# Kernel tuning notes

Measured on AMD Instinct MI355X. Metric: run time of the kernel, lower is better.

The kernel has to match this reference:

```python
import jax, jax.numpy as jnp
import numpy as np

B, T, D = 2, 2048, 2048
H, KV = 16, 4
HD = D // H  # 128
ROPE_BASE = 10000.0


def _rope(t):
    # t: [B, h, T, HD]; faithful to torch apply_rope (even/odd split, concat halves)
    pos = jnp.arange(T, dtype=t.dtype)
    inv_freq = 1.0 / (ROPE_BASE ** (jnp.arange(0, HD, 2, dtype=t.dtype) / HD))
    ang = jnp.einsum('t,f->tf', pos, inv_freq)  # [T, HD/2]
    sin = jnp.sin(ang)[None, None]
    cos = jnp.cos(ang)[None, None]
    t1, t2 = t[..., ::2], t[..., 1::2]
    return jnp.concatenate([t1 * cos - t2 * sin, t1 * sin + t2 * cos], axis=-1)


def setup_inputs() -> dict:
    key = jax.random.key(0)
    kx, kq, kk, kv, ko = jax.random.split(key, 5)
    x = jax.random.normal(kx, (B, T, D), dtype=jnp.float32)
    s = 0.02
    Wq = jax.random.normal(kq, (D, D), dtype=jnp.float32) * s
    Wk = jax.random.normal(kk, (D, KV * HD), dtype=jnp.float32) * s
    Wv = jax.random.normal(kv, (D, KV * HD), dtype=jnp.float32) * s
    Wo = jax.random.normal(ko, (D, D), dtype=jnp.float32) * s
    return {"x": x, "Wq": Wq, "Wk": Wk, "Wv": Wv, "Wo": Wo}


def reference(x, Wq, Wk, Wv, Wo):
    # projections (nn.Linear, no bias)
    q = (x @ Wq).reshape(B, T, H, HD).transpose(0, 2, 1, 3)    # [B,H,T,HD]
    k = (x @ Wk).reshape(B, T, KV, HD).transpose(0, 2, 1, 3)   # [B,KV,T,HD]
    v = (x @ Wv).reshape(B, T, KV, HD).transpose(0, 2, 1, 3)
    q = _rope(q)
    k = _rope(k)
    # GQA: repeat_interleave kv heads to full head count
    g = H // KV
    k = jnp.repeat(k, g, axis=1)
    v = jnp.repeat(v, g, axis=1)
    # causal SDPA, default scale 1/sqrt(head_dim)
    scale = 1.0 / jnp.sqrt(jnp.array(HD, dtype=x.dtype))
    scores = jnp.einsum('bhqd,bhkd->bhqk', q, k) * scale
    mask = jnp.tril(jnp.ones((T, T), dtype=bool))
    scores = jnp.where(mask, scores, jnp.finfo(scores.dtype).min)
    attn = jax.nn.softmax(scores, axis=-1)
    out = jnp.einsum('bhqk,bhkd->bhqd', attn, v)               # [B,H,T,HD]
    out = out.transpose(0, 2, 1, 3).reshape(B, T, D)
    return out @ Wo
```

## Files before the change

### kernel.cpp

```cpp
#include <hip/hip_runtime.h>
#include <math.h>

#define BB 2
#define TT 2048
#define DD 2048
#define HH 16
#define KVHN 4
#define HDIM 128
#define NKV 3072

typedef unsigned short u16;
typedef unsigned int u32;
typedef __bf16 bf16x8 __attribute__((ext_vector_type(8)));
typedef float  f32x4  __attribute__((ext_vector_type(4)));

#define AS1 __attribute__((address_space(1)))
#define AS3 __attribute__((address_space(3)))

__device__ __forceinline__ void dma16(const u16* g, u16* l) {
  __builtin_amdgcn_global_load_lds((const AS1 u32*)g, (AS3 u32*)l, 16, 0, 0);
}

__device__ __forceinline__ u16 f2bf(float f) {
  u32 u = __float_as_uint(f);
  u32 r = (u + 0x7FFFu + ((u >> 16) & 1u)) >> 16;
  return (u16)r;
}
__device__ __forceinline__ float bf2f(u32 h) { return __uint_as_float(h << 16); }

__device__ __forceinline__ u32 pack2(float a, float b) {
  union { __bf16 h[2]; u32 u; } cv;
  cv.h[0] = (__bf16)a; cv.h[1] = (__bf16)b;
  return cv.u;
}

__global__ __launch_bounds__(256) void castf2b(const float* __restrict__ in,
                                               u16* __restrict__ out) {
  size_t i4 = (size_t)blockIdx.x * 256 + threadIdx.x;
  float4 v = *(const float4*)(in + i4 * 4);
  ushort4 o;
  o.x = f2bf(v.x); o.y = f2bf(v.y); o.z = f2bf(v.z); o.w = f2bf(v.w);
  *(ushort4*)(out + i4 * 4) = o;
}

__global__ __launch_bounds__(256) void tcast(const float* __restrict__ W,
                                             u16* __restrict__ WT,
                                             int K, int N) {
  __shared__ float tile[32][33];
  const int n0 = blockIdx.x * 32, k0 = blockIdx.y * 32;
  const int r = threadIdx.x >> 3;
  const int c4 = (threadIdx.x & 7) * 4;
  float4 v = *(const float4*)(W + (size_t)(k0 + r) * N + n0 + c4);
  tile[r][c4 + 0] = v.x; tile[r][c4 + 1] = v.y;
  tile[r][c4 + 2] = v.z; tile[r][c4 + 3] = v.w;
  __syncthreads();
  ushort4 o;
  o.x = f2bf(tile[c4 + 0][r]); o.y = f2bf(tile[c4 + 1][r]);
  o.z = f2bf(tile[c4 + 2][r]); o.w = f2bf(tile[c4 + 3][r]);
  *(ushort4*)(WT + (size_t)(n0 + r) * K + k0 + c4) = o;
}

template <int OUT_BF16>
__global__ __launch_bounds__(256) void gemm2(const u16* __restrict__ A,
                                             const u16* __restrict__ BT,
                                             void* __restrict__ Cv,
                                             int N, int K) {
  __shared__ u16 As[128 * 32];
  __shared__ u16 Bs[128 * 32];
  const int t = threadIdx.x;
  const int l = t & 63, w = t >> 6;
  const int lm = l & 15, quad = l >> 4;
  const int wm = w & 1, wn = w >> 1;
  const int m0 = blockIdx.y * 128, n0 = blockIdx.x * 128;
  const int wu = __builtin_amdgcn_readfirstlane(w);

  f32x4 acc[4][4];
  #pragma unroll
  for (int i = 0; i < 4; ++i)
    #pragma unroll
    for (int j = 0; j < 4; ++j) acc[i][j] = (f32x4){0.f, 0.f, 0.f, 0.f};

  for (int k0 = 0; k0 < K; k0 += 32) {
    __syncthreads();
    #pragma unroll
    for (int i = 0; i < 2; ++i) {
      int p0 = (wu * 2 + i) * 64;
      int p = p0 + l;
      int row = p >> 2, c = p & 3;
      dma16(A  + (size_t)(m0 + row) * K + k0 + c * 8, &As[p0 * 8]);
      dma16(BT + (size_t)(n0 + row) * K + k0 + c * 8, &Bs[p0 * 8]);
    }
    __syncthreads();
    bf16x8 a[4], bq[4];
    #pragma unroll
    for (int i = 0; i < 4; ++i)
      a[i] = *(const bf16x8*)&As[(wm * 64 + i * 16 + lm) * 32 + quad * 8];
    #pragma unroll
    for (int j = 0; j < 4; ++j)
      bq[j] = *(const bf16x8*)&Bs[(wn * 64 + j * 16 + lm) * 32 + quad * 8];
    #pragma unroll
    for (int i = 0; i < 4; ++i)
      #pragma unroll
      for (int j = 0; j < 4; ++j)
        acc[i][j] = __builtin_amdgcn_mfma_f32_16x16x32_bf16(a[i], bq[j], acc[i][j], 0, 0, 0);
  }

  #pragma unroll
  for (int i = 0; i < 4; ++i) {
    #pragma unroll
    for (int r = 0; r < 4; ++r) {
      size_t gr = (size_t)(m0 + wm * 64 + i * 16 + quad * 4 + r);
      #pragma unroll
      for (int j = 0; j < 4; ++j) {
        int gc = n0 + wn * 64 + j * 16 + lm;
        if (OUT_BF16) ((u16*)Cv)[gr * N + gc] = f2bf(acc[i][j][r]);
        else          ((float*)Cv)[gr * N + gc] = acc[i][j][r];
      }
    }
  }
}

__global__ __launch_bounds__(256) void rope2(u16* p) {
  const int row = blockIdx.x;
  const int pos = row & (TT - 1);
  u16* base = p + (size_t)row * NKV;
  float e0[5], e1[5];
  #pragma unroll
  for (int i = 0; i < 5; ++i) {
    int item = threadIdx.x + i * 256;
    int h20 = item >> 6, f = item & 63;
    int col = (h20 < 16) ? h20 * 128 : 2048 + (h20 - 16) * 128;
    u32 u = *(const u32*)(base + col + 2 * f);
    e0[i] = bf2f(u & 0xffffu);
    e1[i] = bf2f(u >> 16);
  }
  __syncthreads();
  #pragma unroll
  for (int i = 0; i < 5; ++i) {
    int item = threadIdx.x + i * 256;
    int h20 = item >> 6, f = item & 63;
    int col = (h20 < 16) ? h20 * 128 : 2048 + (h20 - 16) * 128;
    float sc = (h20 < 16) ? 0.08838834764831845f : 1.0f;
    float inv = exp2f((float)f * -0.20762050593046898f);
    float ang = (float)pos * inv;
    float sn = sinf(ang), cs = cosf(ang);
    base[col + f]      = f2bf((e0[i] * cs - e1[i] * sn) * sc);
    base[col + 64 + f] = f2bf((e0[i] * sn + e1[i] * cs) * sc);
  }
}

__global__ __launch_bounds__(256) void vtrans(const u16* __restrict__ QKV,
                                              u16* __restrict__ Vt) {
  __shared__ u16 tl[64][72];
  const int t0 = blockIdx.x * 64;
  const int y  = blockIdx.y;
  const int b  = blockIdx.z;
  #pragma unroll
  for (int i = 0; i < 2; ++i) {
    int idx = threadIdx.x + i * 256;
    int r = idx >> 3, c = (idx & 7) * 8;
    *(uint4*)&tl[r][c] =
        *(const uint4*)(QKV + (size_t)(b * TT + t0 + r) * NKV + 2560 + y * 64 + c);
  }
  __syncthreads();
  const int vh = y >> 1;
  #pragma unroll
  for (int i = 0; i < 2; ++i) {
    int idx = threadIdx.x + i * 256;
    int dr = idx >> 3, tc = (idx & 7) * 8;
    u16 tmp[8];
    #pragma unroll
    for (int j = 0; j < 8; ++j) tmp[j] = tl[tc + j][dr];
    int dloc = (y & 1) * 64 + dr;
    *(uint4*)(Vt + (size_t)((b * KVHN + vh) * HDIM + dloc) * TT + t0 + tc) =
        *(const uint4*)tmp;
  }
}

__global__ __launch_bounds__(256, 2) void attn2(const u16* __restrict__ QKV,
                                                const u16* __restrict__ Vt,
                                                u16* __restrict__ Ob) {
  __shared__ u16 KsA[64 * 128], KsB[64 * 128];
  __shared__ u16 VsA[128 * 64], VsB[128 * 64];
  __shared__ u16 Pw[4 * 2048];
  const int t = threadIdx.x;
  const int l = t & 63, w = t >> 6;
  const int lm = l & 15, quad = l >> 4;
  const int px = blockIdx.x, h = blockIdx.y, b = blockIdx.z;
  const int kvh = h >> 2;
  const int qlo = px * 64, qhi = (31 - px) * 64;
  const int last = 31 - px;
  const int wu = __builtin_amdgcn_readfirstlane(w);
  u16* pwv = &Pw[w * 2048];
  constexpr float L2E = 1.4426950408889634f;

  bf16x8 qf[2][4];
  {
    size_t r0 = (size_t)(b * TT + qlo + w * 16 + lm) * NKV + h * HDIM;
    size_t r1 = (size_t)(b * TT + qhi + w * 16 + lm) * NKV + h * HDIM;
    #pragma unroll
    for (int ks = 0; ks < 4; ++ks) {
      qf[0][ks] = *(const bf16x8*)(QKV + r0 + ks * 32 + quad * 8);
      qf[1][ks] = *(const bf16x8*)(QKV + r1 + ks * 32 + quad * 8);
    }
  }

  f32x4 o[8][2];
  #pragma unroll
  for (int i = 0; i < 8; ++i)
    #pragma unroll
    for (int n = 0; n < 2; ++n) o[i][n] = (f32x4){0.f, 0.f, 0.f, 0.f};
  float m_[2] = {-1e30f, -1e30f}, l_[2] = {0.f, 0.f};

  auto stageK = [&](int kt, u16* dst) {
    #pragma unroll
    for (int i = 0; i < 4; ++i) {
      int p0 = (wu * 4 + i) * 64;
      int p = p0 + l;
      int row = p >> 4, cp = p & 15, cl = cp ^ (row & 15);
      dma16(QKV + (size_t)(b * TT + kt * 64 + row) * NKV + 2048 + kvh * HDIM + cl * 8,
            dst + p0 * 8);
    }
  };
  auto stageV = [&](int kt, u16* dst) {
    #pragma unroll
    for (int i = 0; i < 4; ++i) {
      int p0 = (wu * 4 + i) * 64;
      int p = p0 + l;
      int d = p >> 3, cp = p & 7, cl = cp ^ (d & 7);
      dma16(Vt + (size_t)((b * KVHN + kvh) * HDIM + d) * TT + kt * 64 + cl * 8,
            dst + p0 * 8);
    }
  };

  auto body = [&](int kt, u16* kcur, u16* vcur, u16* knext, u16* vnext) {
    __syncthreads();
    const bool pf = kt < last;
    if (pf) stageV(kt + 1, vnext);
    const bool lo = (kt <= px);

    f32x4 s[4][2];
    #pragma unroll
    for (int mt = 0; mt < 4; ++mt) {
      s[mt][0] = (f32x4){0.f, 0.f, 0.f, 0.f};
      s[mt][1] = (f32x4){0.f, 0.f, 0.f, 0.f};
    }
    #pragma unroll
    for (int ks = 0; ks < 4; ++ks) {
      #pragma unroll
      for (int mt = 0; mt < 4; ++mt) {
        bf16x8 kb = *(const bf16x8*)&kcur[(mt * 16 + lm) * 128 + (((ks * 4 + quad) ^ lm) * 8)];
        if (lo) s[mt][0] = __builtin_amdgcn_mfma_f32_16x16x32_bf16(kb, qf[0][ks], s[mt][0], 0, 0, 0);
        s[mt][1] = __builtin_amdgcn_mfma_f32_16x16x32_bf16(kb, qf[1][ks], s[mt][1], 0, 0, 0);
      }
    }
    if (pf) stageK(kt + 1, knext);

    if (kt == px) {
      #pragma unroll
      for (int mt = 0; mt < 4; ++mt)
        #pragma unroll
        for (int r = 0; r < 4; ++r) {
          int kv = kt * 64 + mt * 16 + quad * 4 + r;
          if (kv > qlo + w * 16 + lm) s[mt][0][r] = -1e30f;
        }
    }
    if (kt == last) {
      #pragma unroll
      for (int mt = 0; mt < 4; ++mt)
        #pragma unroll
        for (int r = 0; r < 4; ++r) {
          int kv = kt * 64 + mt * 16 + quad * 4 + r;
          if (kv > qhi + w * 16 + lm) s[mt][1][r] = -1e30f;
        }
    }

    float al[2] = {1.f, 1.f};
    #pragma unroll
    for (int nt = 0; nt < 2; ++nt) {
      if (nt == 0 && !lo) continue;
      float mx = -1e30f;
      #pragma unroll
      for (int mt = 0; mt < 4; ++mt)
        #pragma unroll
        for (int r = 0; r < 4; ++r) mx = fmaxf(mx, s[mt][nt][r]);
      mx = fmaxf(mx, __shfl_xor(mx, 16));
      mx = fmaxf(mx, __shfl_xor(mx, 32));
      float mn = fmaxf(m_[nt], mx);
      al[nt] = exp2f((m_[nt] - mn) * L2E);
      m_[nt] = mn;
      float sum = 0.f;
      #pragma unroll
      for (int mt = 0; mt < 4; ++mt)
        #pragma unroll
        for (int r = 0; r < 4; ++r) {
          float pv = exp2f((s[mt][nt][r] - mn) * L2E);
          s[mt][nt][r] = pv;
          sum += pv;
        }
      sum += __shfl_xor(sum, 16);
      sum += __shfl_xor(sum, 32);
      l_[nt] = l_[nt] * al[nt] + sum;

      #pragma unroll
      for (int mt = 0; mt < 4; ++mt) {
        u32 p01 = pack2(s[mt][nt][0], s[mt][nt][1]);
        u32 p23 = pack2(s[mt][nt][2], s[mt][nt][3]);
        int phys = (mt * 2 + (quad >> 1)) ^ (lm & 7);
        int addr = (nt * 16 + lm) * 64 + phys * 8 + (quad & 1) * 4;
        uint2 uv; uv.x = p01; uv.y = p23;
        *(uint2*)&pwv[addr] = uv;
      }
      if (__any(al[nt] < 1.0f)) {
        #pragma unroll
        for (int mt2 = 0; mt2 < 8; ++mt2)
          #pragma unroll
          for (int r = 0; r < 4; ++r) o[mt2][nt][r] *= al[nt];
      }
    }

    #pragma unroll
    for (int ks2 = 0; ks2 < 2; ++ks2) {
      int coff = ((ks2 * 4 + quad) ^ (lm & 7)) * 8;
      bf16x8 pb0, pb1;
      if (lo) pb0 = *(const bf16x8*)&pwv[lm * 64 + coff];
      pb1 = *(const bf16x8*)&pwv[(16 + lm) * 64 + coff];
      #pragma unroll
      for (int mt2 = 0; mt2 < 8; ++mt2) {
        bf16x8 vb = *(const bf16x8*)&vcur[(mt2 * 16 + lm) * 64 + coff];
        if (lo) o[mt2][0] = __builtin_amdgcn_mfma_f32_16x16x32_bf16(vb, pb0, o[mt2][0], 0, 0, 0);
        o[mt2][1] = __builtin_amdgcn_mfma_f32_16x16x32_bf16(vb, pb1, o[mt2][1], 0, 0, 0);
      }
    }
  };

  stageK(0, KsA); stageV(0, VsA);
  for (int kt = 0; kt <= last; ++kt) {
    if ((kt & 1) == 0) body(kt, KsA, VsA, KsB, VsB);
    else               body(kt, KsB, VsB, KsA, VsA);
  }

  #pragma unroll
  for (int nt = 0; nt < 2; ++nt) {
    float inv = 1.f / l_[nt];
    #pragma unroll
    for (int mt2 = 0; mt2 < 8; ++mt2) {
      u32 a0 = pack2(o[mt2][nt][0] * inv, o[mt2][nt][1] * inv);
      u32 a1 = pack2(o[mt2][nt][2] * inv, o[mt2][nt][3] * inv);
      int phys = (mt2 * 2 + (quad >> 1)) ^ (lm & 7);
      int addr = lm * 128 + phys * 8 + (quad & 1) * 4;
      uint2 uv; uv.x = a0; uv.y = a1;
      *(uint2*)&pwv[addr] = uv;
    }
    int qt0 = nt ? qhi : qlo;
    #pragma unroll
    for (int i = 0; i < 4; ++i) {
      int p = i * 64 + l;
      int row = p >> 4, cl = p & 15;
      int cph = cl ^ (row & 7);
      uint4 val = *(const uint4*)&pwv[row * 128 + cph * 8];
      *(uint4*)(Ob + (size_t)(b * TT + qt0 + w * 16 + row) * DD + h * HDIM + cl * 8) = val;
    }
  }
}

extern "C" void kernel_launch(void* const* d_in, const int* in_sizes, int n_in,
                              void* d_out, int out_size, void* d_ws, size_t ws_size,
                              hipStream_t stream) {
  const float* x  = (const float*)d_in[0];
  const float* Wq = (const float*)d_in[1];
  const float* Wk = (const float*)d_in[2];
  const float* Wv = (const float*)d_in[3];
  const float* Wo = (const float*)d_in[4];
  float* out = (float*)d_out;

  u16* xb    = (u16*)d_ws;
  u16* WqkvT = xb + 8388608;
  u16* WoT   = xb + 14680064;
  u16* Vt    = WqkvT;
  u16* Ob    = xb;
  u16* QKVb  = (u16*)d_out;

  dim3 blk(256);
  castf2b<<<8192, blk, 0, stream>>>(x, xb);
  tcast<<<dim3(64, 64), blk, 0, stream>>>(Wq, WqkvT, DD, DD);
  tcast<<<dim3(16, 64), blk, 0, stream>>>(Wk, WqkvT + (size_t)2048 * DD, DD, 512);
  tcast<<<dim3(16, 64), blk, 0, stream>>>(Wv, WqkvT + (size_t)2560 * DD, DD, 512);
  tcast<<<dim3(64, 64), blk, 0, stream>>>(Wo, WoT, DD, DD);

  gemm2<1><<<dim3(NKV / 128, 32), blk, 0, stream>>>(xb, WqkvT, QKVb, NKV, DD);
  rope2<<<BB * TT, blk, 0, stream>>>(QKVb);
  vtrans<<<dim3(32, 8, BB), blk, 0, stream>>>(QKVb, Vt);
  attn2<<<dim3(16, HH, BB), blk, 0, stream>>>(QKVb, Vt, Ob);
  gemm2<0><<<dim3(DD / 128, 32), blk, 0, stream>>>(Ob, WoT, out, DD, DD);
}
```

Before: 333.3 us.

## Restructure attention to one q-tile per block with smaller KV tiles

Replaces the paired low/high q-tile attention kernel with one that processes a single 64-row q tile per block, using 32-row KV tiles and smaller shared buffers so four blocks can reside per CU. Block-to-q-tile mapping is staggered by head to balance causal work. It also adds a lazy max-rescale threshold, MFMA priority hints, precomputed DMA pointers, and sincosf in rope. The aim is higher occupancy and better latency hiding, traded against more blocks with unequal work and more barriers per processed key.

```diff
diff --git a/kernel.cpp b/kernel.cpp
--- a/kernel.cpp
+++ b/kernel.cpp
@@ -143,7 +143,8 @@
     float sc = (h20 < 16) ? 0.08838834764831845f : 1.0f;
     float inv = exp2f((float)f * -0.20762050593046898f);
     float ang = (float)pos * inv;
-    float sn = sinf(ang), cs = cosf(ang);
+    float sn, cs;
+    sincosf(ang, &sn, &cs);
     base[col + f]      = f2bf((e0[i] * cs - e1[i] * sn) * sc);
     base[col + 64 + f] = f2bf((e0[i] * sn + e1[i] * cs) * sc);
   }
@@ -177,190 +178,176 @@
   }
 }
 
-__global__ __launch_bounds__(256, 2) void attn2(const u16* __restrict__ QKV,
+__global__ __launch_bounds__(256, 4) void attn3(const u16* __restrict__ QKV,
                                                 const u16* __restrict__ Vt,
                                                 u16* __restrict__ Ob) {
-  __shared__ u16 KsA[64 * 128], KsB[64 * 128];
-  __shared__ u16 VsA[128 * 64], VsB[128 * 64];
-  __shared__ u16 Pw[4 * 2048];
+  __shared__ u16 KsA[32 * 128], KsB[32 * 128];
+  __shared__ u16 VsA[128 * 32], VsB[128 * 32];
+  __shared__ u16 Pw[4 * 512];
   const int t = threadIdx.x;
   const int l = t & 63, w = t >> 6;
   const int lm = l & 15, quad = l >> 4;
-  const int px = blockIdx.x, h = blockIdx.y, b = blockIdx.z;
+  const int h = blockIdx.y, b = blockIdx.z;
+  const int qbase = (blockIdx.x + (blockIdx.y & 7)) & 31;
+  const int qt = (blockIdx.y & 8) ? (31 - qbase) : qbase;
   const int kvh = h >> 2;
-  const int qlo = px * 64, qhi = (31 - px) * 64;
-  const int last = 31 - px;
+  const int q0 = qt * 64;
+  const int last = 2 * qt + 1;
   const int wu = __builtin_amdgcn_readfirstlane(w);
-  u16* pwv = &Pw[w * 2048];
+  u16* pwv = &Pw[w * 512];
   constexpr float L2E = 1.4426950408889634f;
 
-  bf16x8 qf[2][4];
+  bf16x8 qf[4];
   {
-    size_t r0 = (size_t)(b * TT + qlo + w * 16 + lm) * NKV + h * HDIM;
-    size_t r1 = (size_t)(b * TT + qhi + w * 16 + lm) * NKV + h * HDIM;
-    #pragma unroll
-    for (int ks = 0; ks < 4; ++ks) {
-      qf[0][ks] = *(const bf16x8*)(QKV + r0 + ks * 32 + quad * 8);
-      qf[1][ks] = *(const bf16x8*)(QKV + r1 + ks * 32 + quad * 8);
-    }
-  }
-
-  f32x4 o[8][2];
-  #pragma unroll
-  for (int i = 0; i < 8; ++i)
-    #pragma unroll
-    for (int n = 0; n < 2; ++n) o[i][n] = (f32x4){0.f, 0.f, 0.f, 0.f};
-  float m_[2] = {-1e30f, -1e30f}, l_[2] = {0.f, 0.f};
-
-  auto stageK = [&](int kt, u16* dst) {
-    #pragma unroll
-    for (int i = 0; i < 4; ++i) {
-      int p0 = (wu * 4 + i) * 64;
-      int p = p0 + l;
-      int row = p >> 4, cp = p & 15, cl = cp ^ (row & 15);
-      dma16(QKV + (size_t)(b * TT + kt * 64 + row) * NKV + 2048 + kvh * HDIM + cl * 8,
-            dst + p0 * 8);
-    }
-  };
-  auto stageV = [&](int kt, u16* dst) {
-    #pragma unroll
-    for (int i = 0; i < 4; ++i) {
-      int p0 = (wu * 4 + i) * 64;
-      int p = p0 + l;
-      int d = p >> 3, cp = p & 7, cl = cp ^ (d & 7);
-      dma16(Vt + (size_t)((b * KVHN + kvh) * HDIM + d) * TT + kt * 64 + cl * 8,
-            dst + p0 * 8);
-    }
-  };
-
-  auto body = [&](int kt, u16* kcur, u16* vcur, u16* knext, u16* vnext) {
+    size_t r0 = (size_t)(b * TT + q0 + w * 16 + lm) * NKV + h * HDIM;
+    #pragma unroll
+    for (int ks = 0; ks < 4; ++ks)
+      qf[ks] = *(const bf16x8*)(QKV + r0 + ks * 32 + quad * 8);
+  }
+
+  f32x4 o[8];
+  #pragma unroll
+  for (int i = 0; i < 8; ++i) o[i] = (f32x4){0.f, 0.f, 0.f, 0.f};
+  float m_ = -1e30f, l_ = 0.f;
+
+  const u16 *kg[2], *vg[2];
+  int koff[2], voff[2];
+  #pragma unroll
+  for (int i = 0; i < 2; ++i) {
+    int p0 = (wu * 2 + i) * 64, p = p0 + l;
+    int krow = p >> 4, kcp = p & 15, kcl = kcp ^ (krow & 15);
+    kg[i] = QKV + (size_t)(b * TT + krow) * NKV + 2048 + kvh * HDIM + kcl * 8;
+    koff[i] = p0 * 8;
+    int vd = p >> 2, vcp = p & 3, vcl = vcp ^ (vd & 3);
+    vg[i] = Vt + (size_t)((b * KVHN + kvh) * HDIM + vd) * TT + vcl * 8;
+    voff[i] = p0 * 8;
+  }
+
+  #pragma unroll
+  for (int i = 0; i < 2; ++i) {
+    dma16(kg[i], KsA + koff[i]);
+    dma16(vg[i], VsA + voff[i]);
+    kg[i] += 32 * NKV;
+    vg[i] += 32;
+  }
+
+  const int qrow = q0 + w * 16 + lm;
+
+  auto body = [&](int kt, const u16* kcur, const u16* vcur, u16* knx, u16* vnx) {
     __syncthreads();
     const bool pf = kt < last;
-    if (pf) stageV(kt + 1, vnext);
-    const bool lo = (kt <= px);
-
-    f32x4 s[4][2];
-    #pragma unroll
-    for (int mt = 0; mt < 4; ++mt) {
-      s[mt][0] = (f32x4){0.f, 0.f, 0.f, 0.f};
-      s[mt][1] = (f32x4){0.f, 0.f, 0.f, 0.f};
-    }
+    if (pf) {
+      #pragma unroll
+      for (int i = 0; i < 2; ++i) dma16(vg[i], vnx + voff[i]);
+    }
+
+    f32x4 s[2];
+    s[0] = (f32x4){0.f, 0.f, 0.f, 0.f};
+    s[1] = (f32x4){0.f, 0.f, 0.f, 0.f};
+    __builtin_amdgcn_s_setprio(1);
     #pragma unroll
     for (int ks = 0; ks < 4; ++ks) {
       #pragma unroll
-      for (int mt = 0; mt < 4; ++mt) {
+      for (int mt = 0; mt < 2; ++mt) {
         bf16x8 kb = *(const bf16x8*)&kcur[(mt * 16 + lm) * 128 + (((ks * 4 + quad) ^ lm) * 8)];
-        if (lo) s[mt][0] = __builtin_amdgcn_mfma_f32_16x16x32_bf16(kb, qf[0][ks], s[mt][0], 0, 0, 0);
-        s[mt][1] = __builtin_amdgcn_mfma_f32_16x16x32_bf16(kb, qf[1][ks], s[mt][1], 0, 0, 0);
+        s[mt] = __builtin_amdgcn_mfma_f32_16x16x32_bf16(kb, qf[ks], s[mt], 0, 0, 0);
       }
     }
-    if (pf) stageK(kt + 1, knext);
-
-    if (kt == px) {
-      #pragma unroll
-      for (int mt = 0; mt < 4; ++mt)
+    __builtin_amdgcn_s_setprio(0);
+    if (pf) {
+      #pragma unroll
+      for (int i = 0; i < 2; ++i) {
+        dma16(kg[i], knx + koff[i]);
+        kg[i] += 32 * NKV;
+        vg[i] += 32;
+      }
+    }
+
+    if (kt >= 2 * qt) {
+      #pragma unroll
+      for (int mt = 0; mt < 2; ++mt)
         #pragma unroll
         for (int r = 0; r < 4; ++r) {
-          int kv = kt * 64 + mt * 16 + quad * 4 + r;
-          if (kv > qlo + w * 16 + lm) s[mt][0][r] = -1e30f;
+          int kv = kt * 32 + mt * 16 + quad * 4 + r;
+          if (kv > qrow) s[mt][r] = -1e30f;
         }
     }
-    if (kt == last) {
-      #pragma unroll
-      for (int mt = 0; mt < 4; ++mt)
+
+    float mx = -1e30f;
+    #pragma unroll
+    for (int mt = 0; mt < 2; ++mt)
+      #pragma unroll
+      for (int r = 0; r < 4; ++r) mx = fmaxf(mx, s[mt][r]);
+    mx = fmaxf(mx, __shfl_xor(mx, 16));
+    mx = fmaxf(mx, __shfl_xor(mx, 32));
+    bool upd = mx > m_ + 8.f;
+    float mn = upd ? mx : m_;
+    float al = upd ? exp2f((m_ - mn) * L2E) : 1.f;
+    m_ = mn;
+    float sum = 0.f;
+    #pragma unroll
+    for (int mt = 0; mt < 2; ++mt)
+      #pragma unroll
+      for (int r = 0; r < 4; ++r) {
+        float pv = exp2f((s[mt][r] - mn) * L2E);
+        s[mt][r] = pv;
+        sum += pv;
+      }
+    sum += __shfl_xor(sum, 16);
+    sum += __shfl_xor(sum, 32);
+    l_ = l_ * al + sum;
+
+    #pragma unroll
+    for (int mt = 0; mt < 2; ++mt) {
+      u32 p01 = pack2(s[mt][0], s[mt][1]);
+      u32 p23 = pack2(s[mt][2], s[mt][3]);
+      int phys = (mt * 2 + (quad >> 1)) ^ (lm & 3);
+      int addr = lm * 32 + phys * 8 + (quad & 1) * 4;
+      uint2 uv; uv.x = p01; uv.y = p23;
+      *(uint2*)&pwv[addr] = uv;
+    }
+    if (__any(upd)) {
+      #pragma unroll
+      for (int i = 0; i < 8; ++i)
         #pragma unroll
-        for (int r = 0; r < 4; ++r) {
-          int kv = kt * 64 + mt * 16 + quad * 4 + r;
-          if (kv > qhi + w * 16 + lm) s[mt][1][r] = -1e30f;
-        }
-    }
-
-    float al[2] = {1.f, 1.f};
-    #pragma unroll
-    for (int nt = 0; nt < 2; ++nt) {
-      if (nt == 0 && !lo) continue;
-      float mx = -1e30f;
-      #pragma unroll
-      for (int mt = 0; mt < 4; ++mt)
-        #pragma unroll
-        for (int r = 0; r < 4; ++r) mx = fmaxf(mx, s[mt][nt][r]);
-      mx = fmaxf(mx, __shfl_xor(mx, 16));
-      mx = fmaxf(mx, __shfl_xor(mx, 32));
-      float mn = fmaxf(m_[nt], mx);
-      al[nt] = exp2f((m_[nt] - mn) * L2E);
-      m_[nt] = mn;
-      float sum = 0.f;
-      #pragma unroll
-      for (int mt = 0; mt < 4; ++mt)
-        #pragma unroll
-        for (int r = 0; r < 4; ++r) {
-          float pv = exp2f((s[mt][nt][r] - mn) * L2E);
-          s[mt][nt][r] = pv;
-          sum += pv;
-        }
-      sum += __shfl_xor(sum, 16);
-      sum += __shfl_xor(sum, 32);
-      l_[nt] = l_[nt] * al[nt] + sum;
-
-      #pragma unroll
-      for (int mt = 0; mt < 4; ++mt) {
-        u32 p01 = pack2(s[mt][nt][0], s[mt][nt][1]);
-        u32 p23 = pack2(s[mt][nt][2], s[mt][nt][3]);
-        int phys = (mt * 2 + (quad >> 1)) ^ (lm & 7);
-        int addr = (nt * 16 + lm) * 64 + phys * 8 + (quad & 1) * 4;
-        uint2 uv; uv.x = p01; uv.y = p23;
-        *(uint2*)&pwv[addr] = uv;
-      }
-      if (__any(al[nt] < 1.0f)) {
-        #pragma unroll
-        for (int mt2 = 0; mt2 < 8; ++mt2)
-          #pragma unroll
-          for (int r = 0; r < 4; ++r) o[mt2][nt][r] *= al[nt];
-      }
-    }
-
-    #pragma unroll
-    for (int ks2 = 0; ks2 < 2; ++ks2) {
-      int coff = ((ks2 * 4 + quad) ^ (lm & 7)) * 8;
-      bf16x8 pb0, pb1;
-      if (lo) pb0 = *(const bf16x8*)&pwv[lm * 64 + coff];
-      pb1 = *(const bf16x8*)&pwv[(16 + lm) * 64 + coff];
-      #pragma unroll
-      for (int mt2 = 0; mt2 < 8; ++mt2) {
-        bf16x8 vb = *(const bf16x8*)&vcur[(mt2 * 16 + lm) * 64 + coff];
-        if (lo) o[mt2][0] = __builtin_amdgcn_mfma_f32_16x16x32_bf16(vb, pb0, o[mt2][0], 0, 0, 0);
-        o[mt2][1] = __builtin_amdgcn_mfma_f32_16x16x32_bf16(vb, pb1, o[mt2][1], 0, 0, 0);
-      }
-    }
+        for (int r = 0; r < 4; ++r) o[i][r] *= al;
+    }
+
+    int coff = (quad ^ (lm & 3)) * 8;
+    bf16x8 pb = *(const bf16x8*)&pwv[lm * 32 + coff];
+    __builtin_amdgcn_s_setprio(1);
+    #pragma unroll
+    for (int mt2 = 0; mt2 < 8; ++mt2) {
+      bf16x8 vb = *(const bf16x8*)&vcur[(mt2 * 16 + lm) * 32 + coff];
+      o[mt2] = __builtin_amdgcn_mfma_f32_16x16x32_bf16(vb, pb, o[mt2], 0, 0, 0);
+    }
+    __builtin_amdgcn_s_setprio(0);
   };
 
-  stageK(0, KsA); stageV(0, VsA);
   for (int kt = 0; kt <= last; ++kt) {
     if ((kt & 1) == 0) body(kt, KsA, VsA, KsB, VsB);
     else               body(kt, KsB, VsB, KsA, VsA);
   }
 
-  #pragma unroll
-  for (int nt = 0; nt < 2; ++nt) {
-    float inv = 1.f / l_[nt];
-    #pragma unroll
-    for (int mt2 = 0; mt2 < 8; ++mt2) {
-      u32 a0 = pack2(o[mt2][nt][0] * inv, o[mt2][nt][1] * inv);
-      u32 a1 = pack2(o[mt2][nt][2] * inv, o[mt2][nt][3] * inv);
-      int phys = (mt2 * 2 + (quad >> 1)) ^ (lm & 7);
-      int addr = lm * 128 + phys * 8 + (quad & 1) * 4;
-      uint2 uv; uv.x = a0; uv.y = a1;
-      *(uint2*)&pwv[addr] = uv;
-    }
-    int qt0 = nt ? qhi : qlo;
-    #pragma unroll
-    for (int i = 0; i < 4; ++i) {
-      int p = i * 64 + l;
-      int row = p >> 4, cl = p & 15;
-      int cph = cl ^ (row & 7);
-      uint4 val = *(const uint4*)&pwv[row * 128 + cph * 8];
-      *(uint4*)(Ob + (size_t)(b * TT + qt0 + w * 16 + row) * DD + h * HDIM + cl * 8) = val;
-    }
+  __syncthreads();
+  u16* esc = ((w & 2) ? KsB : KsA) + (w & 1) * 2048;
+  float inv = 1.f / l_;
+  #pragma unroll
+  for (int mt2 = 0; mt2 < 8; ++mt2) {
+    u32 a0 = pack2(o[mt2][0] * inv, o[mt2][1] * inv);
+    u32 a1 = pack2(o[mt2][2] * inv, o[mt2][3] * inv);
+    int phys = (mt2 * 2 + (quad >> 1)) ^ (lm & 7);
+    int addr = lm * 128 + phys * 8 + (quad & 1) * 4;
+    uint2 uv; uv.x = a0; uv.y = a1;
+    *(uint2*)&esc[addr] = uv;
+  }
+  #pragma unroll
+  for (int i = 0; i < 4; ++i) {
+    int p = i * 64 + l;
+    int row = p >> 4, cl = p & 15;
+    int cph = cl ^ (row & 7);
+    uint4 val = *(const uint4*)&esc[row * 128 + cph * 8];
+    *(uint4*)(Ob + (size_t)(b * TT + q0 + w * 16 + row) * DD + h * HDIM + cl * 8) = val;
   }
 }
 
@@ -391,6 +378,6 @@
   gemm2<1><<<dim3(NKV / 128, 32), blk, 0, stream>>>(xb, WqkvT, QKVb, NKV, DD);
   rope2<<<BB * TT, blk, 0, stream>>>(QKVb);
   vtrans<<<dim3(32, 8, BB), blk, 0, stream>>>(QKVb, Vt);
-  attn2<<<dim3(16, HH, BB), blk, 0, stream>>>(QKVb, Vt, Ob);
+  attn3<<<dim3(32, HH, BB), blk, 0, stream>>>(QKVb, Vt, Ob);
   gemm2<0><<<dim3(DD / 128, 32), blk, 0, stream>>>(Ob, WoT, out, DD, DD);
 }
```

After: 343.2 us. 1.03x slower.
